# Performance work log

Measured on AMD Instinct MI355X. Metric: run time of the kernel, lower is better.

Reference implementation:

```python
import jax, jax.numpy as jnp
import numpy as np

N = 50000
E = 800000
IN_F, HID, OUT_F = 512, 256, 64
KEEP = 0.5  # Dropout(0.5)


def setup_inputs() -> dict:
    key = jax.random.key(0)
    ks = jax.random.split(key, 7)
    X = jax.random.normal(ks[0], (N, IN_F), dtype=jnp.float32)
    # Xavier-uniform-style init for the two layer weights
    lim1 = float(np.sqrt(6.0 / (IN_F + HID)))
    lim2 = float(np.sqrt(6.0 / (HID + OUT_F)))
    W1 = jax.random.uniform(ks[1], (IN_F, HID), jnp.float32, -lim1, lim1)
    W2 = jax.random.uniform(ks[2], (HID, OUT_F), jnp.float32, -lim2, lim2)
    a_row = jnp.sort(jax.random.randint(ks[3], (E,), 0, N)).astype(jnp.int64)
    a_col = jax.random.randint(ks[4], (E,), 0, N).astype(jnp.int64)
    a_val = jax.random.uniform(ks[5], (E,), jnp.float32)
    drop_mask = jax.random.randint(ks[6], (N, HID), 0, 2).astype(jnp.int32)
    return {"X": X, "W1": W1, "W2": W2, "a_row": a_row, "a_col": a_col,
            "a_val": a_val, "drop_mask": drop_mask}


def _spmm(a_row, a_col, a_val, dense):
    # A @ dense where A is [N, N] sparse in COO form: gather + weighted segment-sum
    msgs = a_val[:, None] * dense[a_col]          # [E, d]
    return jax.ops.segment_sum(msgs, a_row, num_segments=N)


def reference(X, W1, W2, a_row, a_col, a_val, drop_mask):
    # layer 1: feature transform + neighbor aggregation
    h = _spmm(a_row, a_col, a_val, X @ W1)        # [N, HID]
    h = jax.nn.relu(h)
    h = h * drop_mask.astype(h.dtype) * (1.0 / KEEP)  # Dropout(0.5), train mode
    # layer 2
    out = _spmm(a_row, a_col, a_val, h @ W2)      # [N, OUT_F]
    return jax.nn.log_softmax(out, axis=1)
```

## Files before the change

kernel.cpp:

```cpp
#include <hip/hip_runtime.h>
#include <hip/hip_bf16.h>
#include <math.h>

#define NN   50000
#define EE   800000
#define INF  512
#define HIDF 256
#define OUTF 64
#define MTILES (NN/16)

using short8 = __attribute__((ext_vector_type(8))) short;
using short4v = __attribute__((ext_vector_type(4))) short;
using f32x4  = __attribute__((ext_vector_type(4))) float;

static __device__ __forceinline__ short f2bf(float f){
  unsigned u = __builtin_bit_cast(unsigned, f);
  u += 0x7fff + ((u >> 16) & 1);
  return (short)(u >> 16);
}
static __device__ __forceinline__ float bf2f(short s){
  unsigned u = ((unsigned)(unsigned short)s) << 16;
  return __builtin_bit_cast(float, u);
}

__global__ void k_prep(const int* __restrict__ a_row, int* __restrict__ row_ptr,
                       const float* __restrict__ W1, short* __restrict__ W1p,
                       const float* __restrict__ W2, short* __restrict__ W2bT){
  int b = blockIdx.x, tid = threadIdx.x;
  if (b < 196){
    int i = b * 256 + tid;
    if (i > NN) return;
    int lo = 0, hi = EE;
    while (lo < hi){ int mid = (lo + hi) >> 1; if (a_row[mid] < i) lo = mid + 1; else hi = mid; }
    row_ptr[i] = lo;
  } else if (b < 708){
    int idx = (b - 196) * 256 + tid;
    int k = idx >> 8, col = idx & 255;
    int kk = k >> 5, k2 = k & 31;
    W1p[((kk << 8) + col) * 32 + k2] = f2bf(W1[idx]);
  } else {
    int idx = (b - 708) * 256 + tid;
    int k = idx >> 6, n = idx & 63;
    W2bT[n * HIDF + k] = f2bf(W2[idx]);
  }
}

__global__ __launch_bounds__(256, 3) void k_gemm1(const float* __restrict__ X,
                                                  const short* __restrict__ W1p,
                                                  short* __restrict__ XW1b){
  int wave = threadIdx.x >> 6, lane = threadIdx.x & 63;
  int l16 = lane & 15, quad = lane >> 4;
  int m0 = blockIdx.x * 64 + wave * 16;
  int r = min(m0 + l16, NN - 1);
  const float* arow = X + (size_t)r * INF + quad * 8;
  const short* bbase = W1p + l16 * 32 + quad * 8;

  f32x4 acc[16];
  #pragma unroll
  for (int t = 0; t < 16; t++) acc[t] = (f32x4){0.f,0.f,0.f,0.f};

  for (int kk = 0; kk < INF/32; kk++){
    const float4* ap = (const float4*)(arow + kk * 32);
    float4 a0 = ap[0], a1 = ap[1];
    short8 af;
    af[0]=f2bf(a0.x); af[1]=f2bf(a0.y); af[2]=f2bf(a0.z); af[3]=f2bf(a0.w);
    af[4]=f2bf(a1.x); af[5]=f2bf(a1.y); af[6]=f2bf(a1.z); af[7]=f2bf(a1.w);
    const short* bk = bbase + kk * (256*32);
    #pragma unroll
    for (int nt = 0; nt < 16; nt++){
      short8 bf = *(const short8*)(bk + nt * (16*32));
      acc[nt] = __builtin_amdgcn_mfma_f32_16x16x32_bf16(af, bf, acc[nt], 0, 0, 0);
    }
  }
  #pragma unroll
  for (int nt = 0; nt < 16; nt++){
    int col = nt*16 + l16;
    #pragma unroll
    for (int rr = 0; rr < 4; rr++){
      int row = m0 + quad*4 + rr;
      if (row < NN) XW1b[(size_t)row * HIDF + col] = f2bf(acc[nt][rr]);
    }
  }
}

__global__ __launch_bounds__(256) void k_spmm1(const int* __restrict__ row_ptr,
                                               const int* __restrict__ a_col,
                                               const float* __restrict__ a_val,
                                               const short* __restrict__ XW1b,
                                               const int* __restrict__ drop_mask,
                                               short* __restrict__ hb){
  int wave = threadIdx.x >> 6, lane = threadIdx.x & 63;
  int r = blockIdx.x * 4 + wave;
  int s = row_ptr[r], e = row_ptr[r+1];
  int g = lane >> 4;
  int c16 = lane & 15;
  float acc[16];
  #pragma unroll
  for (int j = 0; j < 16; j++) acc[j] = 0.f;

  int i = s + g;
  for (; i + 4 < e; i += 8){
    float v0 = a_val[i];     int c0 = a_col[i];
    float v1 = a_val[i+4];   int c1 = a_col[i+4];
    const short* p0 = XW1b + (size_t)c0 * HIDF + c16 * 16;
    const short* p1 = XW1b + (size_t)c1 * HIDF + c16 * 16;
    short8 x0a = *(const short8*)(p0);
    short8 x0b = *(const short8*)(p0 + 8);
    short8 x1a = *(const short8*)(p1);
    short8 x1b = *(const short8*)(p1 + 8);
    #pragma unroll
    for (int j = 0; j < 8; j++){
      acc[j]   += v0 * bf2f(x0a[j]);  acc[j+8] += v0 * bf2f(x0b[j]);
      acc[j]   += v1 * bf2f(x1a[j]);  acc[j+8] += v1 * bf2f(x1b[j]);
    }
  }
  for (; i < e; i += 4){
    float v = a_val[i];  int c = a_col[i];
    const short* p = XW1b + (size_t)c * HIDF + c16 * 16;
    short8 xa = *(const short8*)(p);
    short8 xb = *(const short8*)(p + 8);
    #pragma unroll
    for (int j = 0; j < 8; j++){
      acc[j] += v * bf2f(xa[j]);  acc[j+8] += v * bf2f(xb[j]);
    }
  }
  #pragma unroll
  for (int j = 0; j < 16; j++){
    acc[j] += __shfl_xor(acc[j], 16);
    acc[j] += __shfl_xor(acc[j], 32);
  }
  if (lane < 16){
    const int* dm = drop_mask + (size_t)r * HIDF + c16 * 16;
    short8 o0, o1;
    #pragma unroll
    for (int j = 0; j < 8; j++){
      o0[j] = f2bf(fmaxf(acc[j],   0.f) * (float)dm[j]   * 2.0f);
      o1[j] = f2bf(fmaxf(acc[j+8], 0.f) * (float)dm[j+8] * 2.0f);
    }
    short* hp = hb + (size_t)r * HIDF + c16 * 16;
    *(short8*)(hp)     = o0;
    *(short8*)(hp + 8) = o1;
  }
}

__global__ __launch_bounds__(256) void k_gemm2(const short* __restrict__ A,
                                               const short* __restrict__ BT,
                                               short* __restrict__ C){
  int wave = threadIdx.x >> 6, lane = threadIdx.x & 63;
  int tile_m = blockIdx.x * 4 + wave;
  if (tile_m >= MTILES) return;
  int m0 = tile_m * 16, l16 = lane & 15, quad = lane >> 4;

  f32x4 acc[4];
  #pragma unroll
  for (int t = 0; t < 4; t++) acc[t] = (f32x4){0.f,0.f,0.f,0.f};

  const short* ar = A + (size_t)(m0 + l16) * HIDF + quad * 8;
  for (int kk = 0; kk < HIDF/32; kk++){
    short8 af = *(const short8*)(ar + kk * 32);
    #pragma unroll
    for (int nt = 0; nt < 4; nt++){
      short8 bf = *(const short8*)(BT + (size_t)(nt*16 + l16) * HIDF + kk*32 + quad*8);
      acc[nt] = __builtin_amdgcn_mfma_f32_16x16x32_bf16(af, bf, acc[nt], 0, 0, 0);
    }
  }
  #pragma unroll
  for (int nt = 0; nt < 4; nt++){
    int col = nt*16 + l16;
    #pragma unroll
    for (int r = 0; r < 4; r++)
      C[(size_t)(m0 + quad*4 + r) * OUTF + col] = f2bf(acc[nt][r]);
  }
}

__global__ __launch_bounds__(256) void k_spmm2_lsm(const int* __restrict__ row_ptr,
                                                   const int* __restrict__ a_col,
                                                   const float* __restrict__ a_val,
                                                   const short* __restrict__ HW2b,
                                                   float* __restrict__ out){
  int wave = threadIdx.x >> 6, lane = threadIdx.x & 63;
  int r = blockIdx.x * 4 + wave;
  int s = row_ptr[r], e = row_ptr[r+1];
  int g = lane >> 4;
  int c4 = lane & 15;
  float acc[4] = {0,0,0,0};

  int i = s + g;
  for (; i + 4 < e; i += 8){
    float v0 = a_val[i];    int c0 = a_col[i];
    float v1 = a_val[i+4];  int c1 = a_col[i+4];
    short4v x0 = *(const short4v*)(HW2b + (size_t)c0 * OUTF + c4 * 4);
    short4v x1 = *(const short4v*)(HW2b + (size_t)c1 * OUTF + c4 * 4);
    #pragma unroll
    for (int j = 0; j < 4; j++){ acc[j] += v0 * bf2f(x0[j]); acc[j] += v1 * bf2f(x1[j]); }
  }
  for (; i < e; i += 4){
    float v = a_val[i];  int c = a_col[i];
    short4v x = *(const short4v*)(HW2b + (size_t)c * OUTF + c4 * 4);
    #pragma unroll
    for (int j = 0; j < 4; j++) acc[j] += v * bf2f(x[j]);
  }
  #pragma unroll
  for (int j = 0; j < 4; j++){
    acc[j] += __shfl_xor(acc[j], 16);
    acc[j] += __shfl_xor(acc[j], 32);
  }
  float m = fmaxf(fmaxf(acc[0], acc[1]), fmaxf(acc[2], acc[3]));
  #pragma unroll
  for (int o = 1; o <= 8; o <<= 1) m = fmaxf(m, __shfl_xor(m, o));
  float ssum = expf(acc[0]-m) + expf(acc[1]-m) + expf(acc[2]-m) + expf(acc[3]-m);
  #pragma unroll
  for (int o = 1; o <= 8; o <<= 1) ssum += __shfl_xor(ssum, o);
  float ls = logf(ssum);
  if (lane < 16){
    float4 o4 = { acc[0]-m-ls, acc[1]-m-ls, acc[2]-m-ls, acc[3]-m-ls };
    *(float4*)(out + (size_t)r * OUTF + c4 * 4) = o4;
  }
}

extern "C" void kernel_launch(void* const* d_in, const int* in_sizes, int n_in,
                              void* d_out, int out_size, void* d_ws, size_t ws_size,
                              hipStream_t stream) {
  const float* X      = (const float*)d_in[0];
  const float* W1     = (const float*)d_in[1];
  const float* W2     = (const float*)d_in[2];
  const int*   a_row  = (const int*)d_in[3];
  const int*   a_col  = (const int*)d_in[4];
  const float* a_val  = (const float*)d_in[5];
  const int*   drop   = (const int*)d_in[6];
  float*       out    = (float*)d_out;

  char* ws = (char*)d_ws;
  int*   row_ptr = (int*)  (ws);
  short* W1p     = (short*)(ws + 200704);
  short* W2bT    = (short*)(ws + 462848);
  short* XW1b    = (short*)(ws + 495616);
  short* hb      = (short*)(ws + 26095616);
  short* HW2b    = (short*)(ws + 51695616);

  k_prep<<<772, 256, 0, stream>>>(a_row, row_ptr, W1, W1p, W2, W2bT);
  k_gemm1<<<(NN + 63)/64, 256, 0, stream>>>(X, W1p, XW1b);
  k_spmm1<<<NN/4, 256, 0, stream>>>(row_ptr, a_col, a_val, XW1b, drop, hb);
  k_gemm2<<<(MTILES + 3)/4, 256, 0, stream>>>(hb, W2bT, HW2b);
  k_spmm2_lsm<<<NN/4, 256, 0, stream>>>(row_ptr, a_col, a_val, HW2b, out);
}
```

Before: 347.5 us.

## Stage W1 tiles into double-buffered LDS via global_load_lds in GEMM1

The first-layer GEMM now copies each 32-deep W1 slice into shared memory with direct global-to-LDS loads, double-buffered, so all four waves share one copy instead of each reading B from global. It also prefetches the next X fragment in registers while the MFMAs of the current step run. This targets redundant global traffic for W1 and exposed load latency. In exchange it adds 32 KB of LDS per block, a barrier every k-step, and drops the min-blocks hint of 3, which may lower occupancy.

```diff
diff --git a/kernel.cpp b/kernel.cpp
--- a/kernel.cpp
+++ b/kernel.cpp
@@ -12,6 +12,9 @@
 using short8 = __attribute__((ext_vector_type(8))) short;
 using short4v = __attribute__((ext_vector_type(4))) short;
 using f32x4  = __attribute__((ext_vector_type(4))) float;
+
+typedef __attribute__((address_space(1))) const void gas_void;
+typedef __attribute__((address_space(3))) void las_void;
 
 static __device__ __forceinline__ short f2bf(float f){
   unsigned u = __builtin_bit_cast(unsigned, f);
@@ -45,33 +48,56 @@
   }
 }
 
-__global__ __launch_bounds__(256, 3) void k_gemm1(const float* __restrict__ X,
-                                                  const short* __restrict__ W1p,
-                                                  short* __restrict__ XW1b){
+__global__ __launch_bounds__(256) void k_gemm1(const float* __restrict__ X,
+                                               const short* __restrict__ W1p,
+                                               short* __restrict__ XW1b){
+  __shared__ short lds[2][256 * 32];
   int wave = threadIdx.x >> 6, lane = threadIdx.x & 63;
   int l16 = lane & 15, quad = lane >> 4;
   int m0 = blockIdx.x * 64 + wave * 16;
   int r = min(m0 + l16, NN - 1);
-  const float* arow = X + (size_t)r * INF + quad * 8;
-  const short* bbase = W1p + l16 * 32 + quad * 8;
+  const float4* ap = (const float4*)(X + (size_t)r * INF + quad * 8);
 
   f32x4 acc[16];
   #pragma unroll
   for (int t = 0; t < 16; t++) acc[t] = (f32x4){0.f,0.f,0.f,0.f};
 
-  for (int kk = 0; kk < INF/32; kk++){
-    const float4* ap = (const float4*)(arow + kk * 32);
-    float4 a0 = ap[0], a1 = ap[1];
+  auto stage = [&](int buf, int kk){
+    const char* src = (const char*)(W1p + kk * (256 * 32));
+    char* dst = (char*)&lds[buf][0];
+    #pragma unroll
+    for (int j = 0; j < 4; j++){
+      int off = wave * 4096 + j * 1024;
+      __builtin_amdgcn_global_load_lds((gas_void*)(src + off + lane * 16),
+                                       (las_void*)(dst + off), 16, 0, 0);
+    }
+  };
+
+  stage(0, 0);
+  float4 a0 = ap[0], a1 = ap[1];
+  __syncthreads();
+
+  for (int kk = 0; kk < 16; kk++){
+    int cur = kk & 1;
+    float4 na0, na1;
+    if (kk < 15){
+      stage(cur ^ 1, kk + 1);
+      na0 = ap[(kk + 1) * 8];
+      na1 = ap[(kk + 1) * 8 + 1];
+    }
     short8 af;
     af[0]=f2bf(a0.x); af[1]=f2bf(a0.y); af[2]=f2bf(a0.z); af[3]=f2bf(a0.w);
     af[4]=f2bf(a1.x); af[5]=f2bf(a1.y); af[6]=f2bf(a1.z); af[7]=f2bf(a1.w);
-    const short* bk = bbase + kk * (256*32);
+    const short* bp = &lds[cur][0] + l16 * 32 + quad * 8;
     #pragma unroll
     for (int nt = 0; nt < 16; nt++){
-      short8 bf = *(const short8*)(bk + nt * (16*32));
+      short8 bf = *(const short8*)(bp + nt * 512);
       acc[nt] = __builtin_amdgcn_mfma_f32_16x16x32_bf16(af, bf, acc[nt], 0, 0, 0);
     }
-  }
+    a0 = na0; a1 = na1;
+    __syncthreads();
+  }
+
   #pragma unroll
   for (int nt = 0; nt < 16; nt++){
     int col = nt*16 + l16;
```

Measured after the change: 321.8 us. -7.4%, faster.
